# Performance work log

Measured on AMD Instinct MI355X. Metric: run time of the kernel, lower is better.

Reference implementation:

```python
import jax, jax.numpy as jnp
import numpy as np

B, HW, ENC, E, D, A, V, L = 64, 14, 2048, 512, 512, 512, 32000, 32
LN_EPS = 1e-5


def setup_inputs() -> dict:
    key = jax.random.key(0)
    ks = jax.random.split(key, 16)
    s = 0.02
    n = lambda k, sh: jax.random.normal(k, sh, jnp.float32)
    encoder_out = n(ks[0], (B, HW, HW, ENC))
    encoded_captions = jax.random.randint(ks[1], (B, L), 0, V)
    caption_lengths = jax.random.randint(ks[2], (B, 1), 2, L + 1)
    caption_lengths = caption_lengths.at[0, 0].set(L)  # ensure max length present
    return dict(
        encoder_out=encoder_out,
        encoded_captions=encoded_captions,
        caption_lengths=caption_lengths,
        emb=n(ks[3], (V, E)) * s,
        W_enc_att=n(ks[4], (A, ENC)) * s, b_enc_att=jnp.zeros((A,)),
        W_dec_att=n(ks[5], (A, D)) * s, b_dec_att=jnp.zeros((A,)),
        W_full_att=n(ks[6], (1, A)) * s, b_full_att=jnp.zeros((1,)),
        W_ih=n(ks[7], (4 * D, E + ENC)) * s, b_ih=jnp.zeros((4 * D,)),
        W_hh=n(ks[8], (4 * D, D)) * s, b_hh=jnp.zeros((4 * D,)),
        g_h=jnp.ones((D,)), be_h=jnp.zeros((D,)),
        g_c=jnp.ones((D,)), be_c=jnp.zeros((D,)),
        W_init_h=n(ks[9], (D, ENC)) * s, b_init_h=jnp.zeros((D,)),
        W_init_c=n(ks[10], (D, ENC)) * s, b_init_c=jnp.zeros((D,)),
        W_beta=n(ks[11], (ENC, D)) * s, b_beta=jnp.zeros((ENC,)),
        W_fc=n(ks[12], (V, D)) * s, b_fc=jnp.zeros((V,)),
    )


def _layer_norm(x, g, b):
    m = x.mean(-1, keepdims=True)
    v = ((x - m) ** 2).mean(-1, keepdims=True)
    return (x - m) / jnp.sqrt(v + LN_EPS) * g + b


def reference(encoder_out, encoded_captions, caption_lengths, emb,
              W_enc_att, b_enc_att, W_dec_att, b_dec_att, W_full_att, b_full_att,
              W_ih, b_ih, W_hh, b_hh, g_h, be_h, g_c, be_c,
              W_init_h, b_init_h, W_init_c, b_init_c, W_beta, b_beta, W_fc, b_fc):
    bsz = encoder_out.shape[0]
    enc_out = encoder_out.reshape(bsz, -1, encoder_out.shape[-1])  # [B,P,ENC]
    lengths = caption_lengths[:, 0]
    order = jnp.argsort(-lengths)  # stable descending sort (matches torch sort)
    lengths = lengths[order]
    enc_out = enc_out[order]
    caps = encoded_captions[order]
    embeds = emb[caps]  # [B,L,E]
    decode_lengths = lengths - 1
    T = caps.shape[1] - 1  # static max(decode_lengths)

    mean_enc = enc_out.mean(axis=1)
    h = _layer_norm(mean_enc @ W_init_h.T + b_init_h, g_h, be_h)
    c = _layer_norm(mean_enc @ W_init_c.T + b_init_c, g_c, be_c)

    att1 = enc_out @ W_enc_att.T + b_enc_att  # [B,P,A] precomputed once
    prev_seq = jnp.swapaxes(embeds[:, :T], 0, 1)  # [T,B,E] teacher-forced inputs
    masks = jnp.arange(T)[:, None] < decode_lengths[None, :]  # [T,B] active rows

    def step(carry, xs):
        h, c = carry
        prev, mask = xs
        # attention
        att2 = h @ W_dec_att.T + b_dec_att  # [B,A]
        e = jax.nn.relu(att1 + att2[:, None, :]) @ W_full_att[0] + b_full_att[0]  # [B,P]
        alpha = jax.nn.softmax(e, axis=1)
        awe = jnp.einsum('bpe,bp->be', enc_out, alpha)  # [B,ENC]
        gate = jax.nn.sigmoid(h @ W_beta.T + b_beta)
        awe = gate * awe
        # LSTM cell
        x = jnp.concatenate([prev, awe], axis=1)  # [B,E+ENC]
        gates = x @ W_ih.T + b_ih + h @ W_hh.T + b_hh
        i, f, g, o = jnp.split(gates, 4, axis=1)
        c_new = jax.nn.sigmoid(f) * c + jax.nn.sigmoid(i) * jnp.tanh(g)
        h_new = jax.nn.sigmoid(o) * jnp.tanh(c_new)
        h_new = _layer_norm(h_new, g_h, be_h)
        c_new = _layer_norm(c_new, g_c, be_c)
        preds = h_new @ W_fc.T + b_fc  # [B,V]; dropout is identity in eval
        m = mask[:, None]
        h = jnp.where(m, h_new, h)  # freeze finished rows (== torch batch shrink)
        c = jnp.where(m, c_new, c)
        return (h, c), (jnp.where(m, preds, 0.0), jnp.where(m, alpha, 0.0))

    (_, _), (preds_t, alphas_t) = jax.lax.scan(step, (h, c), (prev_seq, masks))
    predictions = jnp.swapaxes(preds_t, 0, 1)  # [B,T,V]
    alphas = jnp.swapaxes(alphas_t, 0, 1)      # [B,T,P]
    return predictions, caps, decode_lengths, alphas, order
```

## Files before the change

### kernel.cpp

```cpp
#include <hip/hip_runtime.h>
#include <cfloat>
#include <math.h>

#define B_ 64
#define P_ 196
#define ENC_ 2048
#define D_ 512
#define V_ 32000
#define L_ 32
#define T_ 31

#define OUT_PREDS 0L
#define OUT_CAPS  63488000L
#define OUT_DECL  63490048L
#define OUT_ALPH  63490112L
#define OUT_ORDER 63878976L

typedef __bf16 bf16;
typedef __bf16 bf16x8 __attribute__((ext_vector_type(8)));
typedef __bf16 bf16x4 __attribute__((ext_vector_type(4)));
typedef __bf16 bf16x2 __attribute__((ext_vector_type(2)));
typedef float  f32x4  __attribute__((ext_vector_type(4)));

static __device__ __forceinline__ float sigmoidf_(float x) { return 1.f / (1.f + __expf(-x)); }

__global__ void k_order(const int* __restrict__ cap_len, const int* __restrict__ caps,
                        int* __restrict__ order_i, int* __restrict__ declen_i,
                        int* __restrict__ caps_i, float* __restrict__ out,
                        int* __restrict__ rmap, int* __restrict__ orow, int* __restrict__ mact)
{
    __shared__ int len_s[B_], dl_s[B_];
    __shared__ int Msh;
    int tid = threadIdx.x;
    len_s[tid] = cap_len[tid];
    __syncthreads();
    int li = len_s[tid];
    int pos = 0;
    for (int j = 0; j < B_; ++j) {
        int lj = len_s[j];
        pos += (lj > li) || (lj == li && j < tid);
    }
    order_i[pos]  = tid;
    declen_i[pos] = li - 1;
    dl_s[pos]     = li - 1;
    out[OUT_ORDER + pos] = (float)tid;
    out[OUT_DECL  + pos] = (float)(li - 1);
    for (int l = 0; l < L_; ++l) {
        int tok = caps[tid * L_ + l];
        caps_i[pos * L_ + l] = tok;
        out[OUT_CAPS + pos * L_ + l] = (float)tok;
    }
    __syncthreads();
    int p = tid;
    int off = 0;
    for (int j = 0; j < p; ++j) off += dl_s[j];
    int dl = dl_s[p];
    if (p == B_ - 1) { Msh = off + dl; mact[0] = off + dl; }
    __syncthreads();
    for (int tt = 0; tt < dl; ++tt) {
        rmap[off + tt] = tt * B_ + p;
        orow[off + tt] = p * T_ + tt;
    }
    int ibase = Msh + p * T_ - off;
    for (int tt = dl; tt < T_; ++tt) {
        rmap[ibase + (tt - dl)] = 0;
        orow[ibase + (tt - dl)] = -(p * T_ + tt) - 1;
    }
}

struct CvtSegs { const float* s[2]; bf16* d[2]; long cum[3]; };
__global__ __launch_bounds__(256) void k_cvt_all(CvtSegs cs)
{
    long i8 = ((long)blockIdx.x * 256 + threadIdx.x) * 8;
    if (i8 >= cs.cum[2]) return;
    int k = 0;
    while (i8 >= cs.cum[k + 1]) ++k;
    long loc = i8 - cs.cum[k];
    const float* src = cs.s[k] + loc;
    float4 a = *(const float4*)(src);
    float4 b = *(const float4*)(src + 4);
    bf16x8 v;
    v[0]=(bf16)a.x; v[1]=(bf16)a.y; v[2]=(bf16)a.z; v[3]=(bf16)a.w;
    v[4]=(bf16)b.x; v[5]=(bf16)b.y; v[6]=(bf16)b.z; v[7]=(bf16)b.w;
    *(bf16x8*)(cs.d[k] + loc) = v;
}

template<int MODE>
__global__ __launch_bounds__(256)
void k_packB(const float* __restrict__ s1, const float* __restrict__ s2,
             bf16* __restrict__ dst, int Kv, int Nsp, int Ksp)
{
    const int ntile = blockIdx.x, tid = threadIdx.x;
    long tbase = (long)ntile * Kv * 16;
    const int groups = Kv * 2;
    for (int g = tid; g < groups; g += 256) {
        int kkq = g >> 4, r16 = g & 15;
        int n = ntile * 16 + r16, k0 = kkq * 8;
        const float* src;
        if (MODE == 0)      src = s1 + (long)n * Kv + k0;
        else if (MODE == 1) src = (n < Nsp) ? s1 + (long)n * Kv + k0
                                            : s2 + (long)(n - Nsp) * Kv + k0;
        else                src = (k0 < Ksp) ? s1 + (long)n * Ksp + k0
                                             : s2 + (long)n * (Kv - Ksp) + (k0 - Ksp);
        float4 a = *(const float4*)src;
        float4 b = *(const float4*)(src + 4);
        bf16x8 v;
        v[0]=(bf16)a.x; v[1]=(bf16)a.y; v[2]=(bf16)a.z; v[3]=(bf16)a.w;
        v[4]=(bf16)b.x; v[5]=(bf16)b.y; v[6]=(bf16)b.z; v[7]=(bf16)b.w;
        *(bf16x8*)(dst + tbase + (long)kkq * 128 + r16 * 8) = v;
    }
}

__global__ __launch_bounds__(256)
void k_packA(const bf16* __restrict__ hseq, const int* __restrict__ rmap, bf16* __restrict__ dst)
{
    const int mt = blockIdx.x, tid = threadIdx.x;
    long tbase = (long)mt * 32768;
    for (int g = tid; g < 4096; g += 256) {
        int mi = g >> 10, rem = g & 1023, kkq = rem >> 4, r16 = rem & 15;
        int row = rmap[mt * 64 + mi * 16 + r16];
        bf16x8 v = *(const bf16x8*)(hseq + (long)row * 512 + kkq * 8);
        *(bf16x8*)(dst + tbase + mi * 8192 + (long)kkq * 128 + r16 * 8) = v;
    }
}

__global__ __launch_bounds__(256) void k_cvt_enc(const float* __restrict__ enc,
                                                 const int* __restrict__ order_i,
                                                 bf16* __restrict__ enc_s,
                                                 bf16* __restrict__ enc_pk)
{
    long i = ((long)blockIdx.x * 256 + threadIdx.x) * 8;
    int r = (int)(i >> 11);
    int k0 = (int)(i & 2047);
    int b = (int)(i / ((long)P_ * ENC_));
    long rem = i - (long)b * P_ * ENC_;
    const float* src = enc + (long)order_i[b] * P_ * ENC_ + rem;
    float4 a = *(const float4*)(src);
    float4 c = *(const float4*)(src + 4);
    bf16x8 v;
    v[0]=(bf16)a.x; v[1]=(bf16)a.y; v[2]=(bf16)a.z; v[3]=(bf16)a.w;
    v[4]=(bf16)c.x; v[5]=(bf16)c.y; v[6]=(bf16)c.z; v[7]=(bf16)c.w;
    *(bf16x8*)(enc_s + i) = v;
    *(bf16x8*)(enc_pk + (long)(r >> 4) * 32768 + (long)(k0 >> 3) * 128 + (r & 15) * 8) = v;
}

__global__ __launch_bounds__(256) void k_meanb(const bf16* __restrict__ enc_s, bf16* __restrict__ mean_b)
{
    int b = blockIdx.x, col = blockIdx.y * 256 + threadIdx.x;
    float s = 0.f;
    const bf16* eb = enc_s + (long)b * P_ * ENC_ + col;
    for (int p = 0; p < P_; ++p) s += (float)eb[(long)p * ENC_];
    mean_b[(long)b * ENC_ + col] = (bf16)(s * (1.f / (float)P_));
}

template<int MI, int FUSE, int EPI, int SWZ, int PK, int PA>
__global__ void __launch_bounds__(256)
k_mgemm(const bf16* __restrict__ A, long lda,
        const bf16* __restrict__ B1, const bf16* __restrict__ B2,
        const float* __restrict__ bias,
        float* __restrict__ Cf, bf16* __restrict__ Cb,
        int N, int K, int kspl, int Nsp, int Mtot)
{
    const int tid = threadIdx.x;
    const int lane = tid & 63, w = tid >> 6;
    int mt, nt, z;
    if (SWZ == 0) { mt = blockIdx.x; nt = blockIdx.y; z = blockIdx.z; }
    else          { int o = blockIdx.x; int wg = (o & 7) * 98 + (o >> 3);
                    mt = wg >> 2; nt = wg & 3; z = 0; }
    const int krange = K / kspl;
    const int k0 = z * krange, k1 = k0 + krange;
    const int r16 = lane & 15, kq = lane >> 4;
    const int koff = kq * 8;

    const bf16* Ap[MI];
#pragma unroll
    for (int mi = 0; mi < MI; ++mi) {
        if (PA) Ap[mi] = A + (long)(mt * MI + mi) * ((long)K * 16) + kq * 128 + r16 * 8;
        else    Ap[mi] = A + (long)(mt * (MI * 16) + mi * 16 + r16) * lda + koff;
    }
    const int ncol0 = nt * 128 + w * 32;

    const bf16* Bp[2];
#pragma unroll
    for (int ni = 0; ni < 2; ++ni) {
        if (PK) {
            Bp[ni] = B1 + (long)((ncol0 + ni * 16) >> 4) * ((long)K * 16) + kq * 128 + r16 * 8;
        } else {
            int n = ncol0 + ni * 16 + r16;
            if (FUSE == 1)
                Bp[ni] = (n < Nsp) ? B1 + (long)n * K + koff
                                   : B2 + (long)(n - Nsp) * K + koff;
            else
                Bp[ni] = B1 + (long)n * K + koff;
        }
    }

    auto loadA = [&](int kk, bf16x8* dst) {
#pragma unroll
        for (int mi = 0; mi < MI; ++mi)
            dst[mi] = PA ? *(const bf16x8*)(Ap[mi] + (long)kk * 16)
                         : *(const bf16x8*)(Ap[mi] + kk);
    };
    auto loadB = [&](int kk, bf16x8* dst) {
#pragma unroll
        for (int ni = 0; ni < 2; ++ni)
            dst[ni] = PK ? *(const bf16x8*)(Bp[ni] + (long)kk * 16)
                         : *(const bf16x8*)(Bp[ni] + kk);
    };

    f32x4 acc[MI][2] = {};
    bf16x8 af[MI], bfr[2];
    loadA(k0, af); loadB(k0, bfr);
    for (int kk = k0 + 32; kk < k1; kk += 32) {
        bf16x8 af2[MI], bf2[2];
        loadA(kk, af2); loadB(kk, bf2);
#pragma unroll
        for (int mi = 0; mi < MI; ++mi)
#pragma unroll
            for (int ni = 0; ni < 2; ++ni)
                acc[mi][ni] = __builtin_amdgcn_mfma_f32_16x16x32_bf16(bfr[ni], af[mi], acc[mi][ni], 0, 0, 0);
#pragma unroll
        for (int mi = 0; mi < MI; ++mi) af[mi] = af2[mi];
#pragma unroll
        for (int ni = 0; ni < 2; ++ni) bfr[ni] = bf2[ni];
    }
#pragma unroll
    for (int mi = 0; mi < MI; ++mi)
#pragma unroll
        for (int ni = 0; ni < 2; ++ni)
            acc[mi][ni] = __builtin_amdgcn_mfma_f32_16x16x32_bf16(bfr[ni], af[mi], acc[mi][ni], 0, 0, 0);

#pragma unroll
    for (int mi = 0; mi < MI; ++mi) {
        const int row = mt * (MI * 16) + mi * 16 + r16;
#pragma unroll
        for (int ni = 0; ni < 2; ++ni) {
            const int col = ncol0 + ni * 16 + kq * 4;
            f32x4 v = acc[mi][ni];
            if (EPI == 0) {
                *(f32x4*)(Cf + (long)z * Mtot * N + (long)row * N + col) = v;
            } else {
                f32x4 bv = *(const f32x4*)(bias + col);
                bf16x4 o;
                o[0]=(bf16)(v[0]+bv[0]); o[1]=(bf16)(v[1]+bv[1]);
                o[2]=(bf16)(v[2]+bv[2]); o[3]=(bf16)(v[3]+bv[3]);
                *(bf16x4*)(Cb + (long)row * N + col) = o;
            }
        }
    }
}

__global__ __launch_bounds__(512)
void k_initln(const float* __restrict__ pi,
              const float* __restrict__ b_h, const float* __restrict__ b_c,
              const float* __restrict__ g_h, const float* __restrict__ be_h,
              const float* __restrict__ g_c, const float* __restrict__ be_c,
              bf16* __restrict__ xh, float* __restrict__ cbuf)
{
    int b = blockIdx.x, d = threadIdx.x;
    float yh = pi[(long)b * 1024 + d]       + b_h[d];
    float yc = pi[(long)b * 1024 + 512 + d] + b_c[d];
    __shared__ float r1[512], r2[512], r3[512], r4[512];
    r1[d] = yh; r2[d] = yh * yh; r3[d] = yc; r4[d] = yc * yc;
    __syncthreads();
    for (int s = 256; s > 0; s >>= 1) {
        if (d < s) { r1[d]+=r1[d+s]; r2[d]+=r2[d+s]; r3[d]+=r3[d+s]; r4[d]+=r4[d+s]; }
        __syncthreads();
    }
    float mh = r1[0] * (1.f/512.f), vh = r2[0] * (1.f/512.f) - mh*mh;
    float mc = r3[0] * (1.f/512.f), vc = r4[0] * (1.f/512.f) - mc*mc;
    float hln = (yh - mh) * rsqrtf(vh + 1e-5f) * g_h[d] + be_h[d];
    float cln = (yc - mc) * rsqrtf(vc + 1e-5f) * g_c[d] + be_c[d];
    xh[(long)b * 3072 + 2560 + d] = (bf16)hln;
    cbuf[(long)b * 512 + d] = cln;
}

__global__ __launch_bounds__(512)
void k_attn(const float* __restrict__ att2gate, const float* __restrict__ b_dec,
            const float* __restrict__ b_beta, const float* __restrict__ Wfull,
            const bf16* __restrict__ att1_b, const bf16* __restrict__ enc_s,
            const int* __restrict__ caps_i, const int* __restrict__ declen_i,
            const float* __restrict__ emb,
            bf16* __restrict__ xh, float* __restrict__ out, int t)
{
    const int b = blockIdx.x >> 1, seg = blockIdx.x & 1, tid = threadIdx.x;
    if (t >= declen_i[b]) {
        if (seg == 1 && tid < P_) out[OUT_ALPH + ((long)b * T_ + t) * P_ + tid] = 0.f;
        return;
    }
    __shared__ float att2s[512], wf[512], red[512], alp[P_];
    {
        float s = b_dec[tid];
#pragma unroll
        for (int zz = 0; zz < 4; ++zz) s += att2gate[((long)zz * 64 + b) * 2560 + tid];
        att2s[tid] = s;
        wf[tid] = Wfull[tid];
    }
    __syncthreads();
    float ev = -FLT_MAX;
    if (tid < P_) {
        const bf16* ar = att1_b + ((long)b * P_ + tid) * 512;
        float acc = 0.f;
        for (int a0 = 0; a0 < 512; a0 += 8) {
            bf16x8 v = *(const bf16x8*)(ar + a0);
#pragma unroll
            for (int j = 0; j < 8; ++j)
                acc += fmaxf((float)v[j] + att2s[a0 + j], 0.f) * wf[a0 + j];
        }
        ev = acc;
    }
    red[tid] = ev;
    __syncthreads();
    for (int s = 256; s > 0; s >>= 1) { if (tid < s) red[tid] = fmaxf(red[tid], red[tid + s]); __syncthreads(); }
    float mx = red[0];
    __syncthreads();
    float ex = (tid < P_) ? __expf(ev - mx) : 0.f;
    red[tid] = ex;
    __syncthreads();
    for (int s = 256; s > 0; s >>= 1) { if (tid < s) red[tid] += red[tid + s]; __syncthreads(); }
    float inv = 1.f / red[0];
    if (tid < P_) alp[tid] = ex * inv;
    __syncthreads();
    if (seg == 1 && tid < P_)
        out[OUT_ALPH + ((long)b * T_ + t) * P_ + tid] = alp[tid];
    const int c0 = seg * 1024 + tid * 2;
    const bf16* eb = enc_s + (long)b * P_ * ENC_ + c0;
    float a0 = 0.f, a1 = 0.f;
#pragma unroll 4
    for (int p = 0; p < P_; ++p) {
        bf16x2 v = *(const bf16x2*)(eb + (long)p * ENC_);
        float al = alp[p];
        a0 += al * (float)v[0]; a1 += al * (float)v[1];
    }
    float g0 = b_beta[c0], g1 = b_beta[c0 + 1];
#pragma unroll
    for (int zz = 0; zz < 4; ++zz) {
        const float* gs = att2gate + ((long)zz * 64 + b) * 2560 + 512 + c0;
        g0 += gs[0]; g1 += gs[1];
    }
    bf16x2 o;
    o[0] = (bf16)(a0 * sigmoidf_(g0));
    o[1] = (bf16)(a1 * sigmoidf_(g1));
    *(bf16x2*)(xh + (long)b * 3072 + 512 + c0) = o;
    if (seg == 0) {
        int tok = caps_i[b * L_ + t];
        xh[(long)b * 3072 + tid] = (bf16)emb[(long)tok * 512 + tid];
    }
}

__global__ __launch_bounds__(512)
void k_lstm(const float* __restrict__ gp, const float* __restrict__ b_ih, const float* __restrict__ b_hh,
            const float* __restrict__ g_h, const float* __restrict__ be_h,
            const float* __restrict__ g_c, const float* __restrict__ be_c,
            bf16* __restrict__ xh, float* __restrict__ cbuf, bf16* __restrict__ hseq,
            const int* __restrict__ declen_i, int t)
{
    int b = blockIdx.x, d = threadIdx.x;
    if (t >= declen_i[b]) return;
    float iv = b_ih[d]        + b_hh[d];
    float fv = b_ih[512 + d]  + b_hh[512 + d];
    float gv = b_ih[1024 + d] + b_hh[1024 + d];
    float ov = b_ih[1536 + d] + b_hh[1536 + d];
#pragma unroll
    for (int s = 0; s < 8; ++s) {
        const float* gs = gp + ((long)s * B_ + b) * 2048;
        iv += gs[d]; fv += gs[512 + d]; gv += gs[1024 + d]; ov += gs[1536 + d];
    }
    float cn = sigmoidf_(fv) * cbuf[(long)b * 512 + d] + sigmoidf_(iv) * tanhf(gv);
    float hn = sigmoidf_(ov) * tanhf(cn);
    __shared__ float r1[512], r2[512], r3[512], r4[512];
    r1[d] = hn; r2[d] = hn * hn; r3[d] = cn; r4[d] = cn * cn;
    __syncthreads();
    for (int s = 256; s > 0; s >>= 1) {
        if (d < s) { r1[d]+=r1[d+s]; r2[d]+=r2[d+s]; r3[d]+=r3[d+s]; r4[d]+=r4[d+s]; }
        __syncthreads();
    }
    float mh = r1[0] * (1.f/512.f), vh = r2[0] * (1.f/512.f) - mh*mh;
    float mc = r3[0] * (1.f/512.f), vc = r4[0] * (1.f/512.f) - mc*mc;
    float hln = (hn - mh) * rsqrtf(vh + 1e-5f) * g_h[d] + be_h[d];
    float cln = (cn - mc) * rsqrtf(vc + 1e-5f) * g_c[d] + be_c[d];
    bf16 hv = (bf16)hln;
    xh[(long)b * 3072 + 2560 + d] = hv;
    hseq[((long)t * B_ + b) * 512 + d] = hv;
    cbuf[(long)b * 512 + d] = cln;
}

__global__ __launch_bounds__(256)
void k_preds(const bf16* __restrict__ Apk, const bf16* __restrict__ Bpk,
             const float* __restrict__ bias, const int* __restrict__ orow,
             const int* __restrict__ mact, float* __restrict__ out)
{
    int o = blockIdx.x; int xcd = o & 7;
    int base = xcd < 6 ? xcd * 969 : 5814 + (xcd - 6) * 968;
    int wg = base + (o >> 3);
    int nt = wg / 31, mt = wg - 31 * nt;
    __shared__ int os[64];
    __shared__ __align__(16) float ct[64][132];
    const int tid = threadIdx.x, lane = tid & 63, w = tid >> 6;
    const int r16 = lane & 15, kq = lane >> 4;
    if (tid < 64) os[tid] = orow[mt * 64 + tid];
    __syncthreads();
    const int r0 = tid >> 5, cc = (tid & 31) * 4;
    const int gcol = nt * 128 + cc;
    if (mt * 64 >= mact[0]) {
        f32x4 zz = {0.f, 0.f, 0.f, 0.f};
#pragma unroll
        for (int it = 0; it < 8; ++it) {
            int r = it * 8 + r0;
            int row = -os[r] - 1;
            *(f32x4*)(out + OUT_PREDS + (long)row * V_ + gcol) = zz;
        }
        return;
    }
    const bf16* Ap[4];
#pragma unroll
    for (int mi = 0; mi < 4; ++mi)
        Ap[mi] = Apk + (long)mt * 32768 + mi * 8192 + kq * 128 + r16 * 8;
    const bf16* Bp[2];
#pragma unroll
    for (int ni = 0; ni < 2; ++ni)
        Bp[ni] = Bpk + (long)((nt * 128 + w * 32 + ni * 16) >> 4) * 8192 + kq * 128 + r16 * 8;

    f32x4 acc[4][2] = {};
    bf16x8 af[4], bfr[2];
#pragma unroll
    for (int mi = 0; mi < 4; ++mi) af[mi] = *(const bf16x8*)(Ap[mi]);
#pragma unroll
    for (int ni = 0; ni < 2; ++ni) bfr[ni] = *(const bf16x8*)(Bp[ni]);
    for (int kk = 32; kk < 512; kk += 32) {
        bf16x8 af2[4], bf2[2];
#pragma unroll
        for (int mi = 0; mi < 4; ++mi) af2[mi] = *(const bf16x8*)(Ap[mi] + kk * 16);
#pragma unroll
        for (int ni = 0; ni < 2; ++ni) bf2[ni] = *(const bf16x8*)(Bp[ni] + kk * 16);
#pragma unroll
        for (int mi = 0; mi < 4; ++mi)
#pragma unroll
            for (int ni = 0; ni < 2; ++ni)
                acc[mi][ni] = __builtin_amdgcn_mfma_f32_16x16x32_bf16(bfr[ni], af[mi], acc[mi][ni], 0, 0, 0);
#pragma unroll
        for (int mi = 0; mi < 4; ++mi) af[mi] = af2[mi];
#pragma unroll
        for (int ni = 0; ni < 2; ++ni) bfr[ni] = bf2[ni];
    }
#pragma unroll
    for (int mi = 0; mi < 4; ++mi)
#pragma unroll
        for (int ni = 0; ni < 2; ++ni)
            acc[mi][ni] = __builtin_amdgcn_mfma_f32_16x16x32_bf16(bfr[ni], af[mi], acc[mi][ni], 0, 0, 0);

#pragma unroll
    for (int mi = 0; mi < 4; ++mi)
#pragma unroll
        for (int ni = 0; ni < 2; ++ni)
            *(f32x4*)&ct[mi * 16 + r16][w * 32 + ni * 16 + kq * 4] = acc[mi][ni];
    __syncthreads();
    f32x4 bv = *(const f32x4*)(bias + gcol);
    f32x4 zz = {0.f, 0.f, 0.f, 0.f};
#pragma unroll
    for (int it = 0; it < 8; ++it) {
        int r = it * 8 + r0;
        int orv = os[r];
        if (orv >= 0) {
            f32x4 v = *(f32x4*)&ct[r][cc];
            f32x4 oo;
            oo[0] = v[0] + bv[0]; oo[1] = v[1] + bv[1];
            oo[2] = v[2] + bv[2]; oo[3] = v[3] + bv[3];
            *(f32x4*)(out + OUT_PREDS + (long)orv * V_ + gcol) = oo;
        } else {
            int row = -orv - 1;
            *(f32x4*)(out + OUT_PREDS + (long)row * V_ + gcol) = zz;
        }
    }
}

extern "C" void kernel_launch(void* const* d_in, const int* in_sizes, int n_in,
                              void* d_out, int out_size, void* d_ws, size_t ws_size,
                              hipStream_t stream)
{
    const float* enc       = (const float*)d_in[0];
    const int*   caps      = (const int*)  d_in[1];
    const int*   caplen    = (const int*)  d_in[2];
    const float* emb       = (const float*)d_in[3];
    const float* W_enc_att = (const float*)d_in[4];
    const float* b_enc_att = (const float*)d_in[5];
    const float* W_dec_att = (const float*)d_in[6];
    const float* b_dec_att = (const float*)d_in[7];
    const float* W_full    = (const float*)d_in[8];
    const float* W_ih      = (const float*)d_in[10];
    const float* b_ih      = (const float*)d_in[11];
    const float* W_hh      = (const float*)d_in[12];
    const float* b_hh      = (const float*)d_in[13];
    const float* g_h       = (const float*)d_in[14];
    const float* be_h      = (const float*)d_in[15];
    const float* g_c       = (const float*)d_in[16];
    const float* be_c      = (const float*)d_in[17];
    const float* W_init_h  = (const float*)d_in[18];
    const float* b_init_h  = (const float*)d_in[19];
    const float* W_init_c  = (const float*)d_in[20];
    const float* b_init_c  = (const float*)d_in[21];
    const float* W_beta    = (const float*)d_in[22];
    const float* b_beta    = (const float*)d_in[23];
    const float* W_fc      = (const float*)d_in[24];
    const float* b_fc      = (const float*)d_in[25];
    float* out = (float*)d_out;

    char* w = (char*)d_ws;
    auto alloc = [&](size_t bytes) { char* p = w; w += (bytes + 255) & ~(size_t)255; return p; };
    int*   order_i  = (int*)  alloc(B_ * 4);
    int*   declen_i = (int*)  alloc(B_ * 4);
    int*   caps_i   = (int*)  alloc(B_ * L_ * 4);
    int*   rmap     = (int*)  alloc(2048 * 4);
    int*   orow     = (int*)  alloc(2048 * 4);
    int*   mact     = (int*)  alloc(256);
    bf16*  enc_s    = (bf16*) alloc((size_t)B_ * P_ * ENC_ * 2);
    bf16*  enc_pk   = (bf16*) alloc((size_t)B_ * P_ * ENC_ * 2);
    bf16*  mean_b   = (bf16*) alloc((size_t)B_ * ENC_ * 2);
    bf16*  att1_b   = (bf16*) alloc((size_t)B_ * P_ * 512 * 2);
    float* pi       = (float*)alloc((size_t)B_ * 1024 * 4);
    float* cbuf     = (float*)alloc((size_t)B_ * 512 * 4);
    bf16*  xh       = (bf16*) alloc((size_t)B_ * 3072 * 2);
    float* att2gate = (float*)alloc((size_t)4 * B_ * 2560 * 4);
    float* gp       = (float*)alloc((size_t)8 * B_ * 2048 * 4);
    bf16*  hseq     = (bf16*) alloc((size_t)T_ * B_ * 512 * 2);
    bf16*  Apk      = (bf16*) alloc((size_t)31 * 32768 * 2);
    bf16*  W_inh_b  = (bf16*) alloc((size_t)512 * 2048 * 2);
    bf16*  W_inc_b  = (bf16*) alloc((size_t)512 * 2048 * 2);
    bf16*  Wenc_pk  = (bf16*) alloc((size_t)512 * 2048 * 2);
    bf16*  Wab_pk   = (bf16*) alloc((size_t)2560 * 512 * 2);
    bf16*  Wg_pk    = (bf16*) alloc((size_t)2048 * 3072 * 2);
    bf16*  Wfc_pk   = (bf16*) alloc((size_t)32000 * 512 * 2);

    k_order<<<1, B_, 0, stream>>>(caplen, caps, order_i, declen_i, caps_i, out, rmap, orow, mact);
    k_cvt_enc<<<12544, 256, 0, stream>>>(enc, order_i, enc_s, enc_pk);
    k_meanb<<<dim3(B_, 8), 256, 0, stream>>>(enc_s, mean_b);

    CvtSegs cs;
    const float* srcs[2] = {W_init_h, W_init_c};
    bf16* dsts[2] = {W_inh_b, W_inc_b};
    long ns[2] = {512L*2048, 512L*2048};
    long cum = 0;
    for (int i = 0; i < 2; ++i) { cs.s[i] = srcs[i]; cs.d[i] = dsts[i]; cs.cum[i] = cum; cum += ns[i]; }
    cs.cum[2] = cum;
    k_cvt_all<<<(int)((cum / 8 + 255) / 256), 256, 0, stream>>>(cs);

    k_packB<0><<<32, 256, 0, stream>>>(W_enc_att, nullptr, Wenc_pk, 2048, 0, 0);
    k_packB<1><<<160, 256, 0, stream>>>(W_dec_att, W_beta, Wab_pk, 512, 512, 0);
    k_packB<2><<<128, 256, 0, stream>>>(W_ih, W_hh, Wg_pk, 3072, 0, 2560);
    k_packB<0><<<2000, 256, 0, stream>>>(W_fc, nullptr, Wfc_pk, 512, 0, 0);

    k_mgemm<4, 1, 0, 0, 0, 0><<<dim3(1, 8, 1), 256, 0, stream>>>(mean_b, 2048, W_inh_b, W_inc_b,
        nullptr, pi, nullptr, 1024, 2048, 1, 512, 64);
    k_initln<<<B_, 512, 0, stream>>>(pi, b_init_h, b_init_c, g_h, be_h, g_c, be_c, xh, cbuf);

    k_mgemm<4, 0, 1, 1, 1, 1><<<784, 256, 0, stream>>>(enc_pk, 0, Wenc_pk, nullptr,
        b_enc_att, nullptr, att1_b, 512, 2048, 1, 0, 12544);

    for (int t = 0; t < T_; ++t) {
        k_mgemm<4, 0, 0, 0, 1, 0><<<dim3(1, 20, 4), 256, 0, stream>>>(xh + 2560, 3072, Wab_pk, nullptr,
            nullptr, att2gate, nullptr, 2560, 512, 4, 0, 64);
        k_attn<<<128, 512, 0, stream>>>(att2gate, b_dec_att, b_beta, W_full, att1_b, enc_s,
            caps_i, declen_i, emb, xh, out, t);
        k_mgemm<4, 0, 0, 0, 1, 0><<<dim3(1, 16, 8), 256, 0, stream>>>(xh, 3072, Wg_pk, nullptr,
            nullptr, gp, nullptr, 2048, 3072, 8, 0, 64);
        k_lstm<<<B_, 512, 0, stream>>>(gp, b_ih, b_hh, g_h, be_h, g_c, be_c,
            xh, cbuf, hseq, declen_i, t);
    }

    k_packA<<<31, 256, 0, stream>>>(hseq, rmap, Apk);
    k_preds<<<7750, 256, 0, stream>>>(Apk, Wfc_pk, b_fc, orow, mact, out);
}
```

Measured before the change: 2.086 ms.

## Fuse decoder attention/gate matvec into LSTM and init kernels, dropping per-step GEMM

The per-timestep split-K MFMA GEMM that computed h·[W_dec_att; W_beta] is removed. Its work moves into the tail of k_lstm and k_initln as a wave-per-row bf16 matvec over a row-major converted weight copy. This saves one launch per step and the split-K partial-sum traffic in k_attn. The cost is that each of the 64 batch blocks now streams the full 2560x512 weight matrix every step, on only 64 workgroups without matrix cores, which may lengthen the serial LSTM kernel.

```diff
diff --git a/kernel.cpp b/kernel.cpp
--- a/kernel.cpp
+++ b/kernel.cpp
@@ -68,11 +68,11 @@
     }
 }
 
-struct CvtSegs { const float* s[2]; bf16* d[2]; long cum[3]; };
+struct CvtSegs { const float* s[4]; bf16* d[4]; long cum[5]; };
 __global__ __launch_bounds__(256) void k_cvt_all(CvtSegs cs)
 {
     long i8 = ((long)blockIdx.x * 256 + threadIdx.x) * 8;
-    if (i8 >= cs.cum[2]) return;
+    if (i8 >= cs.cum[4]) return;
     int k = 0;
     while (i8 >= cs.cum[k + 1]) ++k;
     long loc = i8 - cs.cum[k];
@@ -88,7 +88,7 @@
 template<int MODE>
 __global__ __launch_bounds__(256)
 void k_packB(const float* __restrict__ s1, const float* __restrict__ s2,
-             bf16* __restrict__ dst, int Kv, int Nsp, int Ksp)
+             bf16* __restrict__ dst, int Kv, int Ksp)
 {
     const int ntile = blockIdx.x, tid = threadIdx.x;
     long tbase = (long)ntile * Kv * 16;
@@ -97,11 +97,9 @@
         int kkq = g >> 4, r16 = g & 15;
         int n = ntile * 16 + r16, k0 = kkq * 8;
         const float* src;
-        if (MODE == 0)      src = s1 + (long)n * Kv + k0;
-        else if (MODE == 1) src = (n < Nsp) ? s1 + (long)n * Kv + k0
-                                            : s2 + (long)(n - Nsp) * Kv + k0;
-        else                src = (k0 < Ksp) ? s1 + (long)n * Ksp + k0
-                                             : s2 + (long)n * (Kv - Ksp) + (k0 - Ksp);
+        if (MODE == 0) src = s1 + (long)n * Kv + k0;
+        else           src = (k0 < Ksp) ? s1 + (long)n * Ksp + k0
+                                        : s2 + (long)n * (Kv - Ksp) + (k0 - Ksp);
         float4 a = *(const float4*)src;
         float4 b = *(const float4*)(src + 4);
         bf16x8 v;
@@ -250,17 +248,37 @@
     }
 }
 
+static __device__ __forceinline__ void att2_mv(const float* h_s, const bf16* Wab_rm,
+                                               float* att2g, int b)
+{
+    const int tid = threadIdx.x;
+    const int lane = tid & 63, wv = tid >> 6;
+    float h8[8];
+#pragma unroll
+    for (int q = 0; q < 8; ++q) h8[q] = h_s[lane * 8 + q];
+    for (int r = wv; r < 2560; r += 8) {
+        bf16x8 w8 = *(const bf16x8*)(Wab_rm + (long)r * 512 + lane * 8);
+        float p = 0.f;
+#pragma unroll
+        for (int q = 0; q < 8; ++q) p += h8[q] * (float)w8[q];
+#pragma unroll
+        for (int off = 32; off > 0; off >>= 1) p += __shfl_xor(p, off);
+        if (lane == 0) att2g[(long)b * 2560 + r] = p;
+    }
+}
+
 __global__ __launch_bounds__(512)
 void k_initln(const float* __restrict__ pi,
               const float* __restrict__ b_h, const float* __restrict__ b_c,
               const float* __restrict__ g_h, const float* __restrict__ be_h,
               const float* __restrict__ g_c, const float* __restrict__ be_c,
-              bf16* __restrict__ xh, float* __restrict__ cbuf)
+              const bf16* __restrict__ Wab_rm,
+              bf16* __restrict__ xh, float* __restrict__ cbuf, float* __restrict__ att2g)
 {
     int b = blockIdx.x, d = threadIdx.x;
     float yh = pi[(long)b * 1024 + d]       + b_h[d];
     float yc = pi[(long)b * 1024 + 512 + d] + b_c[d];
-    __shared__ float r1[512], r2[512], r3[512], r4[512];
+    __shared__ float r1[512], r2[512], r3[512], r4[512], h_s[512];
     r1[d] = yh; r2[d] = yh * yh; r3[d] = yc; r4[d] = yc * yc;
     __syncthreads();
     for (int s = 256; s > 0; s >>= 1) {
@@ -273,10 +291,13 @@
     float cln = (yc - mc) * rsqrtf(vc + 1e-5f) * g_c[d] + be_c[d];
     xh[(long)b * 3072 + 2560 + d] = (bf16)hln;
     cbuf[(long)b * 512 + d] = cln;
+    h_s[d] = hln;
+    __syncthreads();
+    att2_mv(h_s, Wab_rm, att2g, b);
 }
 
 __global__ __launch_bounds__(512)
-void k_attn(const float* __restrict__ att2gate, const float* __restrict__ b_dec,
+void k_attn(const float* __restrict__ att2g, const float* __restrict__ b_dec,
             const float* __restrict__ b_beta, const float* __restrict__ Wfull,
             const bf16* __restrict__ att1_b, const bf16* __restrict__ enc_s,
             const int* __restrict__ caps_i, const int* __restrict__ declen_i,
@@ -289,13 +310,8 @@
         return;
     }
     __shared__ float att2s[512], wf[512], red[512], alp[P_];
-    {
-        float s = b_dec[tid];
-#pragma unroll
-        for (int zz = 0; zz < 4; ++zz) s += att2gate[((long)zz * 64 + b) * 2560 + tid];
-        att2s[tid] = s;
-        wf[tid] = Wfull[tid];
-    }
+    att2s[tid] = att2g[(long)b * 2560 + tid] + b_dec[tid];
+    wf[tid] = Wfull[tid];
     __syncthreads();
     float ev = -FLT_MAX;
     if (tid < P_) {
@@ -332,12 +348,8 @@
         float al = alp[p];
         a0 += al * (float)v[0]; a1 += al * (float)v[1];
     }
-    float g0 = b_beta[c0], g1 = b_beta[c0 + 1];
-#pragma unroll
-    for (int zz = 0; zz < 4; ++zz) {
-        const float* gs = att2gate + ((long)zz * 64 + b) * 2560 + 512 + c0;
-        g0 += gs[0]; g1 += gs[1];
-    }
+    float g0 = b_beta[c0]     + att2g[(long)b * 2560 + 512 + c0];
+    float g1 = b_beta[c0 + 1] + att2g[(long)b * 2560 + 512 + c0 + 1];
     bf16x2 o;
     o[0] = (bf16)(a0 * sigmoidf_(g0));
     o[1] = (bf16)(a1 * sigmoidf_(g1));
@@ -352,8 +364,9 @@
 void k_lstm(const float* __restrict__ gp, const float* __restrict__ b_ih, const float* __restrict__ b_hh,
             const float* __restrict__ g_h, const float* __restrict__ be_h,
             const float* __restrict__ g_c, const float* __restrict__ be_c,
+            const bf16* __restrict__ Wab_rm,
             bf16* __restrict__ xh, float* __restrict__ cbuf, bf16* __restrict__ hseq,
-            const int* __restrict__ declen_i, int t)
+            float* __restrict__ att2g, const int* __restrict__ declen_i, int t)
 {
     int b = blockIdx.x, d = threadIdx.x;
     if (t >= declen_i[b]) return;
@@ -368,7 +381,7 @@
     }
     float cn = sigmoidf_(fv) * cbuf[(long)b * 512 + d] + sigmoidf_(iv) * tanhf(gv);
     float hn = sigmoidf_(ov) * tanhf(cn);
-    __shared__ float r1[512], r2[512], r3[512], r4[512];
+    __shared__ float r1[512], r2[512], r3[512], r4[512], h_s[512];
     r1[d] = hn; r2[d] = hn * hn; r3[d] = cn; r4[d] = cn * cn;
     __syncthreads();
     for (int s = 256; s > 0; s >>= 1) {
@@ -383,6 +396,9 @@
     xh[(long)b * 3072 + 2560 + d] = hv;
     hseq[((long)t * B_ + b) * 512 + d] = hv;
     cbuf[(long)b * 512 + d] = cln;
+    h_s[d] = hln;
+    __syncthreads();
+    att2_mv(h_s, Wab_rm, att2g, b);
 }
 
 __global__ __launch_bounds__(256)
@@ -520,14 +536,14 @@
     float* pi       = (float*)alloc((size_t)B_ * 1024 * 4);
     float* cbuf     = (float*)alloc((size_t)B_ * 512 * 4);
     bf16*  xh       = (bf16*) alloc((size_t)B_ * 3072 * 2);
-    float* att2gate = (float*)alloc((size_t)4 * B_ * 2560 * 4);
+    float* att2g    = (float*)alloc((size_t)B_ * 2560 * 4);
     float* gp       = (float*)alloc((size_t)8 * B_ * 2048 * 4);
     bf16*  hseq     = (bf16*) alloc((size_t)T_ * B_ * 512 * 2);
     bf16*  Apk      = (bf16*) alloc((size_t)31 * 32768 * 2);
     bf16*  W_inh_b  = (bf16*) alloc((size_t)512 * 2048 * 2);
     bf16*  W_inc_b  = (bf16*) alloc((size_t)512 * 2048 * 2);
+    bf16*  Wab_rm   = (bf16*) alloc((size_t)2560 * 512 * 2);
     bf16*  Wenc_pk  = (bf16*) alloc((size_t)512 * 2048 * 2);
-    bf16*  Wab_pk   = (bf16*) alloc((size_t)2560 * 512 * 2);
     bf16*  Wg_pk    = (bf16*) alloc((size_t)2048 * 3072 * 2);
     bf16*  Wfc_pk   = (bf16*) alloc((size_t)32000 * 512 * 2);
 
@@ -536,35 +552,33 @@
     k_meanb<<<dim3(B_, 8), 256, 0, stream>>>(enc_s, mean_b);
 
     CvtSegs cs;
-    const float* srcs[2] = {W_init_h, W_init_c};
-    bf16* dsts[2] = {W_inh_b, W_inc_b};
-    long ns[2] = {512L*2048, 512L*2048};
+    const float* srcs[4] = {W_init_h, W_init_c, W_dec_att, W_beta};
+    bf16* dsts[4] = {W_inh_b, W_inc_b, Wab_rm, Wab_rm + (size_t)512 * 512};
+    long ns[4] = {512L*2048, 512L*2048, 512L*512, 2048L*512};
     long cum = 0;
-    for (int i = 0; i < 2; ++i) { cs.s[i] = srcs[i]; cs.d[i] = dsts[i]; cs.cum[i] = cum; cum += ns[i]; }
-    cs.cum[2] = cum;
+    for (int i = 0; i < 4; ++i) { cs.s[i] = srcs[i]; cs.d[i] = dsts[i]; cs.cum[i] = cum; cum += ns[i]; }
+    cs.cum[4] = cum;
     k_cvt_all<<<(int)((cum / 8 + 255) / 256), 256, 0, stream>>>(cs);
 
-    k_packB<0><<<32, 256, 0, stream>>>(W_enc_att, nullptr, Wenc_pk, 2048, 0, 0);
-    k_packB<1><<<160, 256, 0, stream>>>(W_dec_att, W_beta, Wab_pk, 512, 512, 0);
-    k_packB<2><<<128, 256, 0, stream>>>(W_ih, W_hh, Wg_pk, 3072, 0, 2560);
-    k_packB<0><<<2000, 256, 0, stream>>>(W_fc, nullptr, Wfc_pk, 512, 0, 0);
+    k_packB<0><<<32, 256, 0, stream>>>(W_enc_att, nullptr, Wenc_pk, 2048, 0);
+    k_packB<2><<<128, 256, 0, stream>>>(W_ih, W_hh, Wg_pk, 3072, 2560);
+    k_packB<0><<<2000, 256, 0, stream>>>(W_fc, nullptr, Wfc_pk, 512, 0);
 
     k_mgemm<4, 1, 0, 0, 0, 0><<<dim3(1, 8, 1), 256, 0, stream>>>(mean_b, 2048, W_inh_b, W_inc_b,
         nullptr, pi, nullptr, 1024, 2048, 1, 512, 64);
-    k_initln<<<B_, 512, 0, stream>>>(pi, b_init_h, b_init_c, g_h, be_h, g_c, be_c, xh, cbuf);
+    k_initln<<<B_, 512, 0, stream>>>(pi, b_init_h, b_init_c, g_h, be_h, g_c, be_c,
+        Wab_rm, xh, cbuf, att2g);
 
     k_mgemm<4, 0, 1, 1, 1, 1><<<784, 256, 0, stream>>>(enc_pk, 0, Wenc_pk, nullptr,
         b_enc_att, nullptr, att1_b, 512, 2048, 1, 0, 12544);
 
     for (int t = 0; t < T_; ++t) {
-        k_mgemm<4, 0, 0, 0, 1, 0><<<dim3(1, 20, 4), 256, 0, stream>>>(xh + 2560, 3072, Wab_pk, nullptr,
-            nullptr, att2gate, nullptr, 2560, 512, 4, 0, 64);
-        k_attn<<<128, 512, 0, stream>>>(att2gate, b_dec_att, b_beta, W_full, att1_b, enc_s,
+        k_attn<<<128, 512, 0, stream>>>(att2g, b_dec_att, b_beta, W_full, att1_b, enc_s,
             caps_i, declen_i, emb, xh, out, t);
         k_mgemm<4, 0, 0, 0, 1, 0><<<dim3(1, 16, 8), 256, 0, stream>>>(xh, 3072, Wg_pk, nullptr,
             nullptr, gp, nullptr, 2048, 3072, 8, 0, 64);
         k_lstm<<<B_, 512, 0, stream>>>(gp, b_ih, b_hh, g_h, be_h, g_c, be_c,
-            xh, cbuf, hseq, declen_i, t);
+            Wab_rm, xh, cbuf, hseq, att2g, declen_i, t);
     }
 
     k_packA<<<31, 256, 0, stream>>>(hseq, rmap, Apk);
```

Result: slower. 7.351 ms (+252.3%).
